# Kernel tuning notes

Measured on AMD Instinct MI355X. Metric: run time of the kernel, lower is better.

The kernel has to match this reference:

```python
import jax, jax.numpy as jnp
import numpy as np

D = 448  # state_dim == input_dim == output_dim

def _param(key, shape):
    # matches torch.rand(shape) * 0.1 + 0.001
    return jax.random.uniform(key, shape, dtype=jnp.float32) * 0.1 + 0.001

def setup_inputs() -> dict:
    key = jax.random.key(0)
    ks = jax.random.split(key, 9)
    x = jax.random.normal(ks[0], (8, 4096, D), dtype=jnp.float32)
    return {
        "x": x,
        "W_q": _param(ks[1], (D, D)),
        "W_k": _param(ks[2], (D, D)),
        "W_v": _param(ks[3], (D, D)),
        "W_o": _param(ks[4], (D, D)),
        "SSM_A": _param(ks[5], (D, D)),
        "SSM_B": _param(ks[6], (D, D)),
        "SSM_C": _param(ks[7], (D, D)),
    }

def reference(x, W_q, W_k, W_v, W_o, SSM_A, SSM_B, SSM_C):
    # seq_len=4096 > threshold=256 -> quadratic SSM path.
    # structured_processing's einsum 'bsd,dd->bsd' multiplies elementwise by
    # the diagonal of the matrix; the block loop is redundant, so we apply the
    # diagonal scale over the whole sequence in one fused op.
    q = jnp.einsum('bsi,id->bsd', x, W_q)
    k = jnp.einsum('bsi,id->bsd', x, W_k)
    v = jnp.einsum('bsi,id->bsd', x, W_v)
    ssm = (q * jnp.diagonal(SSM_A)
           + k * jnp.diagonal(SSM_B)
           + v * jnp.diagonal(SSM_C))
    # dropout is identity in eval mode
    return jnp.einsum('bsd,do->bso', ssm, W_o)
```

## Files before the change

kernel.cpp:

```cpp
#include <hip/hip_runtime.h>
#include <hip/hip_bf16.h>

#define DDIM 448
#define NSTEP 14

typedef __hip_bfloat16 bf16;
typedef __attribute__((ext_vector_type(8))) short short8;
typedef __attribute__((ext_vector_type(4))) float f32x4;

__device__ __forceinline__ short bf_bits(float f) {
    bf16 h = __float2bfloat16(f);
    return *reinterpret_cast<short*>(&h);
}

__device__ __forceinline__ void async16(const bf16* g, bf16* l) {
    __builtin_amdgcn_global_load_lds(
        (const __attribute__((address_space(1))) void*)g,
        (__attribute__((address_space(3))) void*)l, 16, 0, 0);
}

__global__ __launch_bounds__(256) void prep_wc(
    const float* __restrict__ Wq, const float* __restrict__ Wk,
    const float* __restrict__ Wv, const float* __restrict__ Wo,
    const float* __restrict__ Ad, const float* __restrict__ Bd,
    const float* __restrict__ Cd, bf16* __restrict__ Wt)
{
    __shared__ __align__(16) bf16 As[64 * 32];
    __shared__ __align__(16) bf16 Bs[64 * 32];
    __shared__ float da[DDIM], db[DDIM], dc[DDIM];

    const int tid  = threadIdx.x;
    const int i0   = blockIdx.x * 64;
    const int o0   = blockIdx.y * 64;
    const int lane = tid & 63;
    const int wid  = tid >> 6;
    const int wm   = wid >> 1, wn = wid & 1;
    const int m_   = lane & 15, kq = lane >> 4;

    for (int d = tid; d < DDIM; d += 256) {
        da[d] = Ad[d * DDIM + d];
        db[d] = Bd[d * DDIM + d];
        dc[d] = Cd[d * DDIM + d];
    }

    const int dr  = tid >> 3;
    const int oc8 = (tid & 7) * 8;
    const int ir  = tid >> 2;
    const int dc8 = (tid & 3) * 8;

    f32x4 acc[2][2] = {};

    f32x4 w0 = *(const f32x4*)(Wo + dr * DDIM + o0 + oc8);
    f32x4 w1 = *(const f32x4*)(Wo + dr * DDIM + o0 + oc8 + 4);
    f32x4 q0 = *(const f32x4*)(Wq + (i0 + ir) * DDIM + dc8);
    f32x4 q1 = *(const f32x4*)(Wq + (i0 + ir) * DDIM + dc8 + 4);
    f32x4 t0 = *(const f32x4*)(Wk + (i0 + ir) * DDIM + dc8);
    f32x4 t1 = *(const f32x4*)(Wk + (i0 + ir) * DDIM + dc8 + 4);
    f32x4 v0 = *(const f32x4*)(Wv + (i0 + ir) * DDIM + dc8);
    f32x4 v1 = *(const f32x4*)(Wv + (i0 + ir) * DDIM + dc8 + 4);

    for (int k0 = 0; k0 < DDIM; k0 += 32) {
        __syncthreads();
        #pragma unroll
        for (int j = 0; j < 4; ++j) {
            As[(oc8 + j) * 32 + dr]     = __float2bfloat16(w0[j]);
            As[(oc8 + 4 + j) * 32 + dr] = __float2bfloat16(w1[j]);
        }
        short8 e;
        #pragma unroll
        for (int j = 0; j < 4; ++j) {
            e[j]     = bf_bits(q0[j] * da[k0 + dc8 + j]
                             + t0[j] * db[k0 + dc8 + j]
                             + v0[j] * dc[k0 + dc8 + j]);
            e[j + 4] = bf_bits(q1[j] * da[k0 + dc8 + 4 + j]
                             + t1[j] * db[k0 + dc8 + 4 + j]
                             + v1[j] * dc[k0 + dc8 + 4 + j]);
        }
        *(short8*)&Bs[ir * 32 + dc8] = e;
        __syncthreads();

        const int kn = (k0 + 32 < DDIM) ? k0 + 32 : 0;
        w0 = *(const f32x4*)(Wo + (kn + dr) * DDIM + o0 + oc8);
        w1 = *(const f32x4*)(Wo + (kn + dr) * DDIM + o0 + oc8 + 4);
        q0 = *(const f32x4*)(Wq + (i0 + ir) * DDIM + kn + dc8);
        q1 = *(const f32x4*)(Wq + (i0 + ir) * DDIM + kn + dc8 + 4);
        t0 = *(const f32x4*)(Wk + (i0 + ir) * DDIM + kn + dc8);
        t1 = *(const f32x4*)(Wk + (i0 + ir) * DDIM + kn + dc8 + 4);
        v0 = *(const f32x4*)(Wv + (i0 + ir) * DDIM + kn + dc8);
        v1 = *(const f32x4*)(Wv + (i0 + ir) * DDIM + kn + dc8 + 4);

        short8 af[2], bfr[2];
        #pragma unroll
        for (int mi = 0; mi < 2; ++mi)
            af[mi] = *(const short8*)&As[(wm * 32 + mi * 16 + m_) * 32 + kq * 8];
        #pragma unroll
        for (int ni = 0; ni < 2; ++ni)
            bfr[ni] = *(const short8*)&Bs[(wn * 32 + ni * 16 + m_) * 32 + kq * 8];
        #pragma unroll
        for (int mi = 0; mi < 2; ++mi)
            #pragma unroll
            for (int ni = 0; ni < 2; ++ni)
                acc[mi][ni] = __builtin_amdgcn_mfma_f32_16x16x32_bf16(
                    af[mi], bfr[ni], acc[mi][ni], 0, 0, 0);
    }

    #pragma unroll
    for (int mi = 0; mi < 2; ++mi)
        #pragma unroll
        for (int ni = 0; ni < 2; ++ni) {
            const int o = o0 + wm * 32 + mi * 16 + kq * 4;
            const int i = i0 + wn * 32 + ni * 16 + m_;
            bf16* dst = Wt + (i >> 5) * (DDIM * 32) + (i & 31);
            #pragma unroll
            for (int r = 0; r < 4; ++r)
                dst[(o + r) * 32] = __float2bfloat16(acc[mi][ni][r]);
        }
}

__global__ __launch_bounds__(512, 2) void gemm_xwc(
    const float* __restrict__ X, const bf16* __restrict__ Wt,
    float* __restrict__ out)
{
    __shared__ __align__(16) char smem[74240];

    const int tid  = threadIdx.x;
    const int lane = tid & 63;
    const int wid  = tid >> 6;
    const int wr   = wid >> 2;
    const int wc   = wid & 3;
    const int m_   = lane & 15;
    const int kq   = lane >> 4;
    const int row0 = blockIdx.x * 128;

    const int ar = tid >> 2;
    const int ac = (tid & 3) * 8;
    const float* agp = X + (row0 + ar) * DDIM + ac;

    const bf16* bgp = Wt + wc * 7 * 512 + lane * 8;

    f32x4 acc[4][7] = {};

    {
        bf16* B0 = (bf16*)(smem + 16384);
        if (wid < 4) {
            #pragma unroll
            for (int j = 0; j < 7; ++j)
                async16(bgp + j * 512, B0 + (wc * 7 + j) * 512);
        }
    }

    f32x4 a0 = *(const f32x4*)(agp);
    f32x4 a1 = *(const f32x4*)(agp + 4);
    {
        bf16* A0 = (bf16*)smem;
        short8 w;
        #pragma unroll
        for (int j = 0; j < 4; ++j) {
            w[j] = bf_bits(a0[j]); w[j + 4] = bf_bits(a1[j]);
        }
        *(short8*)&A0[ar * 32 + ac] = w;
    }
    a0 = *(const f32x4*)(agp + 32);
    a1 = *(const f32x4*)(agp + 36);
    __syncthreads();

    for (int s = 0; s < NSTEP; ++s) {
        const int cur = s & 1, nxt = cur ^ 1;
        const bf16* Ac = (const bf16*)(smem + (cur << 13));
        const bf16* Bc = (const bf16*)(smem + 16384 + cur * 28672);

        if (s + 1 < NSTEP) {
            bf16* An = (bf16*)(smem + (nxt << 13));
            bf16* Bn = (bf16*)(smem + 16384 + nxt * 28672);
            short8 w;
            #pragma unroll
            for (int j = 0; j < 4; ++j) {
                w[j] = bf_bits(a0[j]); w[j + 4] = bf_bits(a1[j]);
            }
            *(short8*)&An[ar * 32 + ac] = w;
            if (wid < 4) {
                const bf16* bsrc = bgp + (s + 1) * (DDIM * 32);
                #pragma unroll
                for (int j = 0; j < 7; ++j)
                    async16(bsrc + j * 512, Bn + (wc * 7 + j) * 512);
            }
            if (s + 2 < NSTEP) {
                const int k2 = (s + 2) * 32;
                a0 = *(const f32x4*)(agp + k2);
                a1 = *(const f32x4*)(agp + k2 + 4);
            }
        }

        short8 af[4], bfr[7];
        #pragma unroll
        for (int mi = 0; mi < 4; ++mi)
            af[mi] = *(const short8*)&Ac[(wr * 64 + mi * 16 + m_) * 32 + kq * 8];
        #pragma unroll
        for (int ni = 0; ni < 7; ++ni)
            bfr[ni] = *(const short8*)&Bc[(wc * 112 + ni * 16 + m_) * 32 + kq * 8];

        #pragma unroll
        for (int mi = 0; mi < 4; ++mi)
            #pragma unroll
            for (int ni = 0; ni < 7; ++ni)
                acc[mi][ni] = __builtin_amdgcn_mfma_f32_16x16x32_bf16(
                    af[mi], bfr[ni], acc[mi][ni], 0, 0, 0);

        __syncthreads();
    }

    float* Cb = (float*)(smem + 16384);
    #pragma unroll
    for (int t = 0; t < 4; ++t) {
        if (wr == (t >> 1)) {
            #pragma unroll
            for (int mi2 = 0; mi2 < 2; ++mi2) {
                const int mi = (t & 1) * 2 + mi2;
                #pragma unroll
                for (int ni = 0; ni < 7; ++ni) {
                    const int col = wc * 112 + ni * 16 + m_;
                    #pragma unroll
                    for (int r = 0; r < 4; ++r)
                        Cb[(mi2 * 16 + kq * 4 + r) * 452 + col] = acc[mi][ni][r];
                }
            }
        }
        __syncthreads();
        const f32x4* Cb4 = (const f32x4*)Cb;
        f32x4* dst4 = (f32x4*)(out + (row0 + t * 32) * DDIM);
        #pragma unroll
        for (int j = 0; j < 7; ++j) {
            const int v   = j * 512 + tid;
            const int row = v / 112;
            const int cw  = v - row * 112;
            dst4[v] = Cb4[row * 113 + cw];
        }
        __syncthreads();
    }
}

extern "C" void kernel_launch(void* const* d_in, const int* in_sizes, int n_in,
                              void* d_out, int out_size, void* d_ws, size_t ws_size,
                              hipStream_t stream) {
    const float* x  = (const float*)d_in[0];
    const float* Wq = (const float*)d_in[1];
    const float* Wk = (const float*)d_in[2];
    const float* Wv = (const float*)d_in[3];
    const float* Wo = (const float*)d_in[4];
    const float* Ad = (const float*)d_in[5];
    const float* Bd = (const float*)d_in[6];
    const float* Cd = (const float*)d_in[7];

    bf16*  Wt  = (bf16*)d_ws;
    float* out = (float*)d_out;

    const int M = in_sizes[0] / DDIM;

    prep_wc<<<dim3(7, 7), 256, 0, stream>>>(Wq, Wk, Wv, Wo, Ad, Bd, Cd, Wt);
    gemm_xwc<<<M / 128, 512, 0, stream>>>(x, Wt, out);
}
```

Measured before the change: 142.8 us.

## Triple-buffer weight tiles with prefetch distance two and explicit vmcnt waits

Moves the async global-to-LDS loads of the weight operand to three LDS buffers, prefetching two k-steps ahead instead of one. __syncthreads is replaced with explicit s_waitcnt vmcnt counts plus s_barrier, so only the oldest outstanding loads must finish before each step. This hides more global load latency. The cost is that LDS grows from about 74KB to 100KB per block, which may reduce blocks per CU below the launch bound of two. The vmcnt counts also have to match the exact number of in-flight loads, including the A-operand register loads.

```diff
diff --git a/kernel.cpp b/kernel.cpp
--- a/kernel.cpp
+++ b/kernel.cpp
@@ -121,7 +121,7 @@
     const float* __restrict__ X, const bf16* __restrict__ Wt,
     float* __restrict__ out)
 {
-    __shared__ __align__(16) char smem[74240];
+    __shared__ __align__(16) char smem[102400];
 
     const int tid  = threadIdx.x;
     const int lane = tid & 63;
@@ -140,15 +140,6 @@
 
     f32x4 acc[4][7] = {};
 
-    {
-        bf16* B0 = (bf16*)(smem + 16384);
-        if (wid < 4) {
-            #pragma unroll
-            for (int j = 0; j < 7; ++j)
-                async16(bgp + j * 512, B0 + (wc * 7 + j) * 512);
-        }
-    }
-
     f32x4 a0 = *(const f32x4*)(agp);
     f32x4 a1 = *(const f32x4*)(agp + 4);
     {
@@ -162,33 +153,47 @@
     }
     a0 = *(const f32x4*)(agp + 32);
     a1 = *(const f32x4*)(agp + 36);
-    __syncthreads();
-
+    if (wid < 4) {
+        bf16* B0 = (bf16*)(smem + 16384);
+        bf16* B1 = (bf16*)(smem + 16384 + 28672);
+        #pragma unroll
+        for (int j = 0; j < 7; ++j)
+            async16(bgp + j * 512, B0 + (wc * 7 + j) * 512);
+        const bf16* b1 = bgp + DDIM * 32;
+        #pragma unroll
+        for (int j = 0; j < 7; ++j)
+            async16(b1 + j * 512, B1 + (wc * 7 + j) * 512);
+    }
+    asm volatile("s_waitcnt vmcnt(7)" ::: "memory");
+    asm volatile("s_waitcnt lgkmcnt(0)" ::: "memory");
+    __builtin_amdgcn_s_barrier();
+
+    int bcur = 0;
+    int bn2  = 2;
     for (int s = 0; s < NSTEP; ++s) {
-        const int cur = s & 1, nxt = cur ^ 1;
-        const bf16* Ac = (const bf16*)(smem + (cur << 13));
-        const bf16* Bc = (const bf16*)(smem + 16384 + cur * 28672);
+        const bf16* Ac = (const bf16*)(smem + ((s & 1) << 13));
+        const bf16* Bc = (const bf16*)(smem + 16384 + bcur * 28672);
 
         if (s + 1 < NSTEP) {
-            bf16* An = (bf16*)(smem + (nxt << 13));
-            bf16* Bn = (bf16*)(smem + 16384 + nxt * 28672);
+            bf16* An = (bf16*)(smem + (((s + 1) & 1) << 13));
             short8 w;
             #pragma unroll
             for (int j = 0; j < 4; ++j) {
                 w[j] = bf_bits(a0[j]); w[j + 4] = bf_bits(a1[j]);
             }
             *(short8*)&An[ar * 32 + ac] = w;
-            if (wid < 4) {
-                const bf16* bsrc = bgp + (s + 1) * (DDIM * 32);
-                #pragma unroll
-                for (int j = 0; j < 7; ++j)
-                    async16(bsrc + j * 512, Bn + (wc * 7 + j) * 512);
-            }
-            if (s + 2 < NSTEP) {
-                const int k2 = (s + 2) * 32;
-                a0 = *(const f32x4*)(agp + k2);
-                a1 = *(const f32x4*)(agp + k2 + 4);
-            }
+        }
+        if (s + 2 < NSTEP) {
+            const int k2 = (s + 2) * 32;
+            a0 = *(const f32x4*)(agp + k2);
+            a1 = *(const f32x4*)(agp + k2 + 4);
+        }
+        if (s + 2 < NSTEP && wid < 4) {
+            bf16* Bn = (bf16*)(smem + 16384 + bn2 * 28672);
+            const bf16* bsrc = bgp + (s + 2) * (DDIM * 32);
+            #pragma unroll
+            for (int j = 0; j < 7; ++j)
+                async16(bsrc + j * 512, Bn + (wc * 7 + j) * 512);
         }
 
         short8 af[4], bfr[7];
@@ -206,7 +211,16 @@
                 acc[mi][ni] = __builtin_amdgcn_mfma_f32_16x16x32_bf16(
                     af[mi], bfr[ni], acc[mi][ni], 0, 0, 0);
 
-        __syncthreads();
+        if (s < NSTEP - 2) {
+            asm volatile("s_waitcnt vmcnt(9)" ::: "memory");
+        } else {
+            asm volatile("s_waitcnt vmcnt(0)" ::: "memory");
+        }
+        asm volatile("s_waitcnt lgkmcnt(0)" ::: "memory");
+        __builtin_amdgcn_s_barrier();
+
+        bcur = (bcur == 2) ? 0 : bcur + 1;
+        bn2  = (bn2  == 2) ? 0 : bn2  + 1;
     }
 
     float* Cb = (float*)(smem + 16384);
```

Measured after the change: 140.1 us. About the same (-1.9%).

## Load weight fragments directly into registers, bypassing LDS staging

Applied to the files above, without the earlier changes.

The weight operand is no longer staged through shared memory with async global-to-LDS copies. Each wave now loads its own MFMA B fragments straight from global memory into double-buffered registers, prefetching one k-step ahead. The main loop is unrolled by two to alternate the register buffers. __syncthreads is replaced with explicit lgkmcnt waits plus raw barriers that do not wait on vector memory. The intent is to cut LDS traffic and barrier cost, in exchange for higher register pressure and global loads that now complete inside the compute loop.

```diff
diff --git a/kernel.cpp b/kernel.cpp
--- a/kernel.cpp
+++ b/kernel.cpp
@@ -11,12 +11,6 @@
 __device__ __forceinline__ short bf_bits(float f) {
     bf16 h = __float2bfloat16(f);
     return *reinterpret_cast<short*>(&h);
-}
-
-__device__ __forceinline__ void async16(const bf16* g, bf16* l) {
-    __builtin_amdgcn_global_load_lds(
-        (const __attribute__((address_space(1))) void*)g,
-        (__attribute__((address_space(3))) void*)l, 16, 0, 0);
 }
 
 __global__ __launch_bounds__(256) void prep_wc(
@@ -136,18 +130,10 @@
     const int ac = (tid & 3) * 8;
     const float* agp = X + (row0 + ar) * DDIM + ac;
 
-    const bf16* bgp = Wt + wc * 7 * 512 + lane * 8;
+    const bf16* bgp = Wt + (wc * 112 + m_) * 32 + kq * 8;
 
     f32x4 acc[4][7] = {};
-
-    {
-        bf16* B0 = (bf16*)(smem + 16384);
-        if (wid < 4) {
-            #pragma unroll
-            for (int j = 0; j < 7; ++j)
-                async16(bgp + j * 512, B0 + (wc * 7 + j) * 512);
-        }
-    }
+    short8 bA[7], bB[7];
 
     f32x4 a0 = *(const f32x4*)(agp);
     f32x4 a1 = *(const f32x4*)(agp + 4);
@@ -162,52 +148,53 @@
     }
     a0 = *(const f32x4*)(agp + 32);
     a1 = *(const f32x4*)(agp + 36);
-    __syncthreads();
-
-    for (int s = 0; s < NSTEP; ++s) {
-        const int cur = s & 1, nxt = cur ^ 1;
-        const bf16* Ac = (const bf16*)(smem + (cur << 13));
-        const bf16* Bc = (const bf16*)(smem + 16384 + cur * 28672);
-
-        if (s + 1 < NSTEP) {
-            bf16* An = (bf16*)(smem + (nxt << 13));
-            bf16* Bn = (bf16*)(smem + 16384 + nxt * 28672);
-            short8 w;
-            #pragma unroll
-            for (int j = 0; j < 4; ++j) {
-                w[j] = bf_bits(a0[j]); w[j + 4] = bf_bits(a1[j]);
-            }
-            *(short8*)&An[ar * 32 + ac] = w;
-            if (wid < 4) {
-                const bf16* bsrc = bgp + (s + 1) * (DDIM * 32);
-                #pragma unroll
-                for (int j = 0; j < 7; ++j)
-                    async16(bsrc + j * 512, Bn + (wc * 7 + j) * 512);
-            }
-            if (s + 2 < NSTEP) {
-                const int k2 = (s + 2) * 32;
-                a0 = *(const f32x4*)(agp + k2);
-                a1 = *(const f32x4*)(agp + k2 + 4);
-            }
-        }
-
-        short8 af[4], bfr[7];
-        #pragma unroll
-        for (int mi = 0; mi < 4; ++mi)
-            af[mi] = *(const short8*)&Ac[(wr * 64 + mi * 16 + m_) * 32 + kq * 8];
-        #pragma unroll
-        for (int ni = 0; ni < 7; ++ni)
-            bfr[ni] = *(const short8*)&Bc[(wc * 112 + ni * 16 + m_) * 32 + kq * 8];
-
-        #pragma unroll
-        for (int mi = 0; mi < 4; ++mi)
-            #pragma unroll
-            for (int ni = 0; ni < 7; ++ni)
-                acc[mi][ni] = __builtin_amdgcn_mfma_f32_16x16x32_bf16(
-                    af[mi], bfr[ni], acc[mi][ni], 0, 0, 0);
-
-        __syncthreads();
-    }
+    #pragma unroll
+    for (int j = 0; j < 7; ++j)
+        bA[j] = *(const short8*)(bgp + j * 512);
+    asm volatile("s_waitcnt lgkmcnt(0)" ::: "memory");
+    __builtin_amdgcn_s_barrier();
+
+#define GSTEP(S, BCUR, BNXT)                                                 \
+    {                                                                        \
+        const bf16* Ac = (const bf16*)(smem + (((S) & 1) << 13));            \
+        if ((S) + 1 < NSTEP) {                                               \
+            const bf16* bs = bgp + ((S) + 1) * (DDIM * 32);                  \
+            _Pragma("unroll")                                                \
+            for (int j = 0; j < 7; ++j)                                      \
+                BNXT[j] = *(const short8*)(bs + j * 512);                    \
+            bf16* An = (bf16*)(smem + ((((S) + 1) & 1) << 13));              \
+            short8 w;                                                        \
+            _Pragma("unroll")                                                \
+            for (int j = 0; j < 4; ++j) {                                    \
+                w[j] = bf_bits(a0[j]); w[j + 4] = bf_bits(a1[j]);            \
+            }                                                                \
+            *(short8*)&An[ar * 32 + ac] = w;                                 \
+        }                                                                    \
+        if ((S) + 2 < NSTEP) {                                               \
+            a0 = *(const f32x4*)(agp + ((S) + 2) * 32);                      \
+            a1 = *(const f32x4*)(agp + ((S) + 2) * 32 + 4);                  \
+        }                                                                    \
+        short8 af[4];                                                        \
+        _Pragma("unroll")                                                    \
+        for (int mi = 0; mi < 4; ++mi)                                       \
+            af[mi] = *(const short8*)&Ac[(wr * 64 + mi * 16 + m_) * 32       \
+                                         + kq * 8];                          \
+        _Pragma("unroll")                                                    \
+        for (int mi = 0; mi < 4; ++mi)                                       \
+            _Pragma("unroll")                                                \
+            for (int ni = 0; ni < 7; ++ni)                                   \
+                acc[mi][ni] = __builtin_amdgcn_mfma_f32_16x16x32_bf16(       \
+                    af[mi], BCUR[ni], acc[mi][ni], 0, 0, 0);                 \
+        asm volatile("s_waitcnt lgkmcnt(0)" ::: "memory");                   \
+        __builtin_amdgcn_s_barrier();                                        \
+    }
+
+    #pragma unroll
+    for (int ss = 0; ss < NSTEP; ss += 2) {
+        GSTEP(ss,     bA, bB)
+        GSTEP(ss + 1, bB, bA)
+    }
+#undef GSTEP
 
     float* Cb = (float*)(smem + 16384);
     #pragma unroll
@@ -225,7 +212,8 @@
                 }
             }
         }
-        __syncthreads();
+        asm volatile("s_waitcnt lgkmcnt(0)" ::: "memory");
+        __builtin_amdgcn_s_barrier();
         const f32x4* Cb4 = (const f32x4*)Cb;
         f32x4* dst4 = (f32x4*)(out + (row0 + t * 32) * DDIM);
         #pragma unroll
@@ -235,7 +223,8 @@
             const int cw  = v - row * 112;
             dst4[v] = Cb4[row * 113 + cw];
         }
-        __syncthreads();
+        asm volatile("s_waitcnt lgkmcnt(0)" ::: "memory");
+        __builtin_amdgcn_s_barrier();
     }
 }
 
```

Result: no change. 145.2 us (+1.7%).
